# Performance work log

Measured on AMD Instinct MI355X. Metric: run time of the kernel, lower is better.

## Reference

```python
import jax, jax.numpy as jnp
import numpy as np

B = 1
NG, NM = 262144, 40962          # grid nodes, mesh nodes (icosphere level 6)
E = 131072                      # grid2mesh edges (g2m_enum)
EM, EM2 = 65536, 65536          # mesh edges / mesh2grid edges (passthrough)
GEMB = MEMB = EEMB = 128
HID1, HID2 = 512, 64
EPS = 1e-5


def setup_inputs() -> dict:
    key = jax.random.key(0)
    ks = jax.random.split(key, 16)
    inp = {
        "gx": jax.random.normal(ks[0], (B, NG, GEMB), jnp.float32),
        "mx": jax.random.normal(ks[1], (B, NM, MEMB), jnp.float32),
        "me_i": jax.random.randint(ks[2], (2, EM), 0, NM, jnp.int64 if jax.config.jax_enable_x64 else jnp.int32),
        "me_x": jax.random.normal(ks[3], (B, EM, EEMB), jnp.float32),
        "g2me_i": jnp.stack([
            jax.random.randint(ks[4], (E,), 0, NG),   # row: grid node index
            jax.random.randint(ks[5], (E,), 0, NM),   # col: mesh node index
        ]),
        "g2me_x": jax.random.normal(ks[6], (B, E, EEMB), jnp.float32),
        "m2ge_i": jax.random.randint(ks[7], (2, EM2), 0, NM),
        "m2ge_x": jax.random.normal(ks[8], (B, EM2, EEMB), jnp.float32),
    }
    # MLP params (Linear stores W as [out, in]; we keep [in, out] for x @ W)
    din = GEMB + MEMB + EEMB
    s1, s2, s3 = 1.0 / np.sqrt(din), 1.0 / np.sqrt(HID1), 1.0 / np.sqrt(HID2)
    inp["W1"] = jax.random.uniform(ks[9], (din, HID1), jnp.float32, -s1, s1)
    inp["b1"] = jax.random.uniform(ks[10], (HID1,), jnp.float32, -s1, s1)
    inp["W2"] = jax.random.uniform(ks[11], (HID1, HID2), jnp.float32, -s2, s2)
    inp["b2"] = jax.random.uniform(ks[12], (HID2,), jnp.float32, -s2, s2)
    inp["W3"] = jax.random.uniform(ks[13], (HID2, EEMB), jnp.float32, -s3, s3)
    inp["b3"] = jax.random.uniform(ks[14], (EEMB,), jnp.float32, -s3, s3)
    # LayerNorm over normalized_shape=(E, EEMB): per-(edge, channel) affine
    inp["ln_w"] = jnp.ones((E, EEMB), jnp.float32)
    inp["ln_b"] = jnp.zeros((E, EEMB), jnp.float32)
    return inp


def reference(gx, mx, me_i, me_x, g2me_i, g2me_x, m2ge_i, m2ge_x,
              W1, b1, W2, b2, W3, b3, ln_w, ln_b):
    row, col = g2me_i[0], g2me_i[1]
    # gather + concat: [B, E, gemb+memb+eemb]
    h = jnp.concatenate([gx[:, row], mx[:, col], g2me_x], axis=-1)
    h = jax.nn.silu(h @ W1 + b1)
    h = jax.nn.silu(h @ W2 + b2)
    h = h @ W3 + b3                                   # [B, E, eemb]
    # LayerNorm over BOTH edge and embed dims (normalized_shape=(E, eemb))
    mean = jnp.mean(h, axis=(-2, -1), keepdims=True)
    var = jnp.mean(jnp.square(h - mean), axis=(-2, -1), keepdims=True)
    h = (h - mean) * jax.lax.rsqrt(var + EPS) * ln_w + ln_b
    g2me_x_new = g2me_x + h
    return g2me_x_new
```

## Files before the change

kernel.cpp:

```cpp
#include <hip/hip_runtime.h>

#define NE    131072
#define DIN   384
#define DH1   512
#define DH2   64

typedef __attribute__((ext_vector_type(8))) short short8_t;
typedef __attribute__((ext_vector_type(4))) float f32x4;
typedef unsigned short ushort_t;

__device__ __forceinline__ float bf2f(ushort_t u) {
  union { unsigned int i; float f; } v; v.i = ((unsigned int)u) << 16; return v.f;
}
__device__ __forceinline__ ushort_t f2bf(float f) {
  union { float f; unsigned int i; } v; v.f = f;
  unsigned int r = v.i + 0x7fff + ((v.i >> 16) & 1);
  return (ushort_t)(r >> 16);
}
__device__ __forceinline__ float silu_f(float x) {
  return x / (1.0f + __expf(-x));
}
__device__ __forceinline__ void wave_fence() {
  __builtin_amdgcn_wave_barrier();
  asm volatile("" ::: "memory");
}

__global__ void prep_kernel(const void* __restrict__ W1, const void* __restrict__ W2,
                            const void* __restrict__ W3, const void* __restrict__ b1,
                            const void* __restrict__ b2, const void* __restrict__ b3,
                            const void* __restrict__ lnw, const void* __restrict__ g2me_raw,
                            ushort_t* __restrict__ W1f, ushort_t* __restrict__ W2f,
                            ushort_t* __restrict__ W3f, float* __restrict__ b1f,
                            float* __restrict__ b2f, float* __restrict__ b3f,
                            float* __restrict__ stats, int* __restrict__ flag,
                            int* __restrict__ idx32) {
  const int isbf = (((const ushort_t*)lnw)[0] == 0x3F80) ? 1 : 0;
  const unsigned int* gi = (const unsigned int*)g2me_raw;
  const int is64 = ((gi[1] | gi[3] | gi[5] | gi[7]) == 0) ? 1 : 0;

  int tid = blockIdx.x * blockDim.x + threadIdx.x;
  int nth = gridDim.x * blockDim.x;
  if (tid == 0) { stats[0] = 0.f; stats[1] = 0.f; *flag = isbf; }

  const ushort_t* W1u = (const ushort_t*)W1; const float* W1p = (const float*)W1;
  const ushort_t* W2u = (const ushort_t*)W2; const float* W2p = (const float*)W2;
  const ushort_t* W3u = (const ushort_t*)W3; const float* W3p = (const float*)W3;
  const ushort_t* b1u = (const ushort_t*)b1; const float* b1p = (const float*)b1;
  const ushort_t* b2u = (const ushort_t*)b2; const float* b2p = (const float*)b2;
  const ushort_t* b3u = (const ushort_t*)b3; const float* b3p = (const float*)b3;

  for (int i = tid; i < DIN * DH1; i += nth) {
    int j = i & 7, l = (i >> 3) & 63, f = i >> 9;
    int kc = f / 48, kt = (f >> 2) % 12, nt = f & 3;
    int col = kc * 64 + nt * 16 + (l & 15);
    int k   = kt * 32 + (l >> 4) * 8 + j;
    int s = k * DH1 + col;
    W1f[i] = isbf ? W1u[s] : f2bf(W1p[s]);
  }
  for (int i = tid; i < DH1 * DH2; i += nth) {
    int j = i & 7, l = (i >> 3) & 63, f = i >> 9;
    int kc = f >> 3, kt2 = (f >> 2) & 1, nt = f & 3;
    int col = nt * 16 + (l & 15);
    int k   = kc * 64 + kt2 * 32 + (l >> 4) * 8 + j;
    int s = k * DH2 + col;
    W2f[i] = isbf ? W2u[s] : f2bf(W2p[s]);
  }
  for (int i = tid; i < DH2 * 128; i += nth) {
    int j = i & 7, l = (i >> 3) & 63, f = i >> 9;
    int nt = f >> 1, kt = f & 1;
    int col = nt * 16 + (l & 15);
    int k   = kt * 32 + (l >> 4) * 8 + j;
    int s = k * 128 + col;
    W3f[i] = isbf ? W3u[s] : f2bf(W3p[s]);
  }
  for (int i = tid; i < DH1; i += nth) b1f[i] = isbf ? bf2f(b1u[i]) : b1p[i];
  for (int i = tid; i < DH2; i += nth) b2f[i] = isbf ? bf2f(b2u[i]) : b2p[i];
  for (int i = tid; i < 128; i += nth) b3f[i] = isbf ? bf2f(b3u[i]) : b3p[i];

  const long long* g64 = (const long long*)g2me_raw;
  const int* g32 = (const int*)g2me_raw;
  for (int i = tid; i < 2 * NE; i += nth)
    idx32[i] = is64 ? (int)g64[i] : g32[i];
}

template <int BF16>
__launch_bounds__(256)
__global__ void mlp_kernel(const void* __restrict__ gx_, const void* __restrict__ mx_,
                           const int* __restrict__ idx, const void* __restrict__ gex_,
                           const ushort_t* __restrict__ W1f, const float* __restrict__ b1f,
                           const ushort_t* __restrict__ W2f, const float* __restrict__ b2f,
                           const ushort_t* __restrict__ W3f, const float* __restrict__ b3f,
                           void* __restrict__ h3g_, float* __restrict__ stats,
                           const int* __restrict__ flag) {
  if (flag[0] != BF16) return;

  __shared__ __align__(16) ushort_t h1c[64][72];
  __shared__ float red[8];

  const int tid  = threadIdx.x;
  const int w    = tid >> 6;
  const int lane = tid & 63;
  const int quad = lane >> 4;
  const int c16  = lane & 15;
  const int e0   = blockIdx.x * 64;
  const int e    = e0 + w * 16 + c16;

  const int r0 = idx[e];
  const int c0 = idx[NE + e];

  short8_t afr[12];
  if (BF16) {
    const ushort_t* pg = (const ushort_t*)gx_  + (size_t)r0 * 128;
    const ushort_t* pm = (const ushort_t*)mx_  + (size_t)c0 * 128;
    const ushort_t* pe = (const ushort_t*)gex_ + (size_t)e  * 128;
    #pragma unroll
    for (int kt = 0; kt < 12; ++kt) {
      const ushort_t* p = (kt < 4) ? pg : (kt < 8) ? pm : pe;
      afr[kt] = *(const short8_t*)(p + (kt & 3) * 32 + quad * 8);
    }
  } else {
    const float* pg = (const float*)gx_  + (size_t)r0 * 128;
    const float* pm = (const float*)mx_  + (size_t)c0 * 128;
    const float* pe = (const float*)gex_ + (size_t)e  * 128;
    #pragma unroll
    for (int kt = 0; kt < 12; ++kt) {
      const float* p = ((kt < 4) ? pg : (kt < 8) ? pm : pe) + (kt & 3) * 32 + quad * 8;
      float4 u = *(const float4*)p;
      float4 v = *(const float4*)(p + 4);
      short8_t s;
      s[0] = (short)f2bf(u.x); s[1] = (short)f2bf(u.y);
      s[2] = (short)f2bf(u.z); s[3] = (short)f2bf(u.w);
      s[4] = (short)f2bf(v.x); s[5] = (short)f2bf(v.y);
      s[6] = (short)f2bf(v.z); s[7] = (short)f2bf(v.w);
      afr[kt] = s;
    }
  }

  const f32x4 vzero = {0.f, 0.f, 0.f, 0.f};
  f32x4 acc2[4];
  #pragma unroll
  for (int nt = 0; nt < 4; ++nt) acc2[nt] = vzero;

  for (int kc = 0; kc < 8; ++kc) {
    f32x4 acc1[4];
    #pragma unroll
    for (int nt = 0; nt < 4; ++nt) acc1[nt] = vzero;
    #pragma unroll
    for (int kt = 0; kt < 12; ++kt) {
      #pragma unroll
      for (int nt = 0; nt < 4; ++nt) {
        short8_t b = *(const short8_t*)(W1f + ((size_t)((kc * 12 + kt) * 4 + nt) * 64 + lane) * 8);
        acc1[nt] = __builtin_amdgcn_mfma_f32_16x16x32_bf16(afr[kt], b, acc1[nt], 0, 0, 0);
      }
    }
    #pragma unroll
    for (int nt = 0; nt < 4; ++nt) {
      float bias = b1f[kc * 64 + nt * 16 + c16];
      #pragma unroll
      for (int r = 0; r < 4; ++r) {
        float x = acc1[nt][r] + bias;
        h1c[w * 16 + quad * 4 + r][nt * 16 + c16] = f2bf(silu_f(x));
      }
    }
    wave_fence();
    #pragma unroll
    for (int kt2 = 0; kt2 < 2; ++kt2) {
      short8_t a2 = *(const short8_t*)&h1c[w * 16 + c16][kt2 * 32 + quad * 8];
      #pragma unroll
      for (int nt = 0; nt < 4; ++nt) {
        short8_t b = *(const short8_t*)(W2f + ((size_t)((kc * 2 + kt2) * 4 + nt) * 64 + lane) * 8);
        acc2[nt] = __builtin_amdgcn_mfma_f32_16x16x32_bf16(a2, b, acc2[nt], 0, 0, 0);
      }
    }
    wave_fence();
  }

  #pragma unroll
  for (int nt = 0; nt < 4; ++nt) {
    float bias = b2f[nt * 16 + c16];
    #pragma unroll
    for (int r = 0; r < 4; ++r) {
      float x = acc2[nt][r] + bias;
      h1c[w * 16 + quad * 4 + r][nt * 16 + c16] = f2bf(silu_f(x));
    }
  }
  wave_fence();
  short8_t a3[2];
  #pragma unroll
  for (int kt = 0; kt < 2; ++kt)
    a3[kt] = *(const short8_t*)&h1c[w * 16 + c16][kt * 32 + quad * 8];

  float s = 0.f, s2 = 0.f;
  #pragma unroll
  for (int nt = 0; nt < 8; ++nt) {
    f32x4 acc3 = vzero;
    #pragma unroll
    for (int kt = 0; kt < 2; ++kt) {
      short8_t b = *(const short8_t*)(W3f + ((size_t)(nt * 2 + kt) * 64 + lane) * 8);
      acc3 = __builtin_amdgcn_mfma_f32_16x16x32_bf16(a3[kt], b, acc3, 0, 0, 0);
    }
    float bias = b3f[nt * 16 + c16];
    #pragma unroll
    for (int r = 0; r < 4; ++r) {
      float v = acc3[r] + bias;
      s += v; s2 += v * v;
      size_t oidx = (size_t)(e0 + w * 16 + quad * 4 + r) * 128 + nt * 16 + c16;
      if (BF16) ((ushort_t*)h3g_)[oidx] = f2bf(v);
      else      ((float*)h3g_)[oidx] = v;
    }
  }

  #pragma unroll
  for (int off = 32; off > 0; off >>= 1) {
    s  += __shfl_xor(s, off, 64);
    s2 += __shfl_xor(s2, off, 64);
  }
  if (lane == 0) { red[w] = s; red[4 + w] = s2; }
  __syncthreads();
  if (tid == 0) {
    atomicAdd(&stats[0], red[0] + red[1] + red[2] + red[3]);
    atomicAdd(&stats[1], red[4] + red[5] + red[6] + red[7]);
  }
}

__device__ __forceinline__ unsigned int ln2(unsigned int h, unsigned int g,
                                            unsigned int wv, unsigned int bv,
                                            float mean, float inv) {
  float h0 = bf2f((ushort_t)(h & 0xffff)), h1 = bf2f((ushort_t)(h >> 16));
  float g0 = bf2f((ushort_t)(g & 0xffff)), g1 = bf2f((ushort_t)(g >> 16));
  float w0 = bf2f((ushort_t)(wv & 0xffff)), w1 = bf2f((ushort_t)(wv >> 16));
  float b0 = bf2f((ushort_t)(bv & 0xffff)), b1 = bf2f((ushort_t)(bv >> 16));
  float r0 = g0 + (h0 - mean) * inv * w0 + b0;
  float r1 = g1 + (h1 - mean) * inv * w1 + b1;
  return (unsigned int)f2bf(r0) | ((unsigned int)f2bf(r1) << 16);
}

template <int BF16>
__global__ void finalize_kernel(const void* __restrict__ gex_, const void* __restrict__ lnw_,
                                const void* __restrict__ lnb_, const float* __restrict__ stats,
                                void* __restrict__ out_, const int* __restrict__ flag) {
  if (flag[0] != BF16) return;
  const float invN = 1.0f / 16777216.0f;
  float mean = stats[0] * invN;
  float var  = stats[1] * invN - mean * mean;
  float inv  = rsqrtf(var + 1e-5f);
  size_t i = ((size_t)blockIdx.x * 256 + threadIdx.x) * 8;

  if (BF16) {
    ushort_t* out = (ushort_t*)out_;
    const ushort_t* gex = (const ushort_t*)gex_;
    const ushort_t* lnw = (const ushort_t*)lnw_;
    const ushort_t* lnb = (const ushort_t*)lnb_;
    uint4 hv = *(const uint4*)(out + i);
    uint4 gv = *(const uint4*)(gex + i);
    uint4 wv = *(const uint4*)(lnw + i);
    uint4 bv = *(const uint4*)(lnb + i);
    uint4 o;
    o.x = ln2(hv.x, gv.x, wv.x, bv.x, mean, inv);
    o.y = ln2(hv.y, gv.y, wv.y, bv.y, mean, inv);
    o.z = ln2(hv.z, gv.z, wv.z, bv.z, mean, inv);
    o.w = ln2(hv.w, gv.w, wv.w, bv.w, mean, inv);
    *(uint4*)(out + i) = o;
  } else {
    float* out = (float*)out_;
    const float* gex = (const float*)gex_;
    const float* lnw = (const float*)lnw_;
    const float* lnb = (const float*)lnb_;
    #pragma unroll
    for (int j = 0; j < 8; j += 4) {
      float4 h = *(const float4*)(out + i + j);
      float4 g = *(const float4*)(gex + i + j);
      float4 w = *(const float4*)(lnw + i + j);
      float4 b = *(const float4*)(lnb + i + j);
      float4 o;
      o.x = g.x + (h.x - mean) * inv * w.x + b.x;
      o.y = g.y + (h.y - mean) * inv * w.y + b.y;
      o.z = g.z + (h.z - mean) * inv * w.z + b.z;
      o.w = g.w + (h.w - mean) * inv * w.w + b.w;
      *(float4*)(out + i + j) = o;
    }
  }
}

extern "C" void kernel_launch(void* const* d_in, const int* in_sizes, int n_in,
                              void* d_out, int out_size, void* d_ws, size_t ws_size,
                              hipStream_t stream) {
  const void* gx     = d_in[0];
  const void* mx     = d_in[1];
  const void* g2me_i = d_in[4];
  const void* gex    = d_in[5];
  const void* W1 = d_in[8];  const void* b1 = d_in[9];
  const void* W2 = d_in[10]; const void* b2 = d_in[11];
  const void* W3 = d_in[12]; const void* b3 = d_in[13];
  const void* lnw = d_in[14]; const void* lnb = d_in[15];

  char* ws = (char*)d_ws;
  ushort_t* W1f = (ushort_t*)(ws);
  ushort_t* W2f = (ushort_t*)(ws + 393216);
  ushort_t* W3f = (ushort_t*)(ws + 458752);
  float*    b1f = (float*)(ws + 475136);
  float*    b2f = (float*)(ws + 477184);
  float*    b3f = (float*)(ws + 477440);
  float*  stats = (float*)(ws + 477952);
  int*     flag = (int*)(ws + 477960);
  int*    idx32 = (int*)(ws + 478208);

  prep_kernel<<<dim3(256), dim3(256), 0, stream>>>(
      W1, W2, W3, b1, b2, b3, lnw, g2me_i,
      W1f, W2f, W3f, b1f, b2f, b3f, stats, flag, idx32);

  mlp_kernel<0><<<dim3(NE / 64), dim3(256), 0, stream>>>(
      gx, mx, idx32, gex, W1f, b1f, W2f, b2f, W3f, b3f, d_out, stats, flag);
  mlp_kernel<1><<<dim3(NE / 64), dim3(256), 0, stream>>>(
      gx, mx, idx32, gex, W1f, b1f, W2f, b2f, W3f, b3f, d_out, stats, flag);

  finalize_kernel<0><<<dim3(8192), dim3(256), 0, stream>>>(
      gex, lnw, lnb, stats, d_out, flag);
  finalize_kernel<1><<<dim3(8192), dim3(256), 0, stream>>>(
      gex, lnw, lnb, stats, d_out, flag);
}
```

Baseline: 758.9 us.

## Process two 16-edge tiles per wave to reuse weight fragments

Each wave now handles 32 edges as two M-tiles, so every W1/W2/W3 fragment loaded from global memory feeds two MFMAs instead of one. This halves the weight-load traffic per edge, and the grid shrinks to NE/128 blocks. The prep kernel's weight swizzle loops now iterate over source indices, so reads are coalesced and writes are scattered. The cost is more registers (two sets of A fragments and accumulators), which launch_bounds(256,2) caps, and a larger shared buffer; spills or lower occupancy are possible.

Measured after the change: 642.7 us. 1.18x faster.

```diff
diff --git a/kernel.cpp b/kernel.cpp
--- a/kernel.cpp
+++ b/kernel.cpp
@@ -49,29 +49,26 @@
   const ushort_t* b2u = (const ushort_t*)b2; const float* b2p = (const float*)b2;
   const ushort_t* b3u = (const ushort_t*)b3; const float* b3p = (const float*)b3;
 
-  for (int i = tid; i < DIN * DH1; i += nth) {
-    int j = i & 7, l = (i >> 3) & 63, f = i >> 9;
-    int kc = f / 48, kt = (f >> 2) % 12, nt = f & 3;
-    int col = kc * 64 + nt * 16 + (l & 15);
-    int k   = kt * 32 + (l >> 4) * 8 + j;
-    int s = k * DH1 + col;
-    W1f[i] = isbf ? W1u[s] : f2bf(W1p[s]);
-  }
-  for (int i = tid; i < DH1 * DH2; i += nth) {
-    int j = i & 7, l = (i >> 3) & 63, f = i >> 9;
-    int kc = f >> 3, kt2 = (f >> 2) & 1, nt = f & 3;
-    int col = nt * 16 + (l & 15);
-    int k   = kc * 64 + kt2 * 32 + (l >> 4) * 8 + j;
-    int s = k * DH2 + col;
-    W2f[i] = isbf ? W2u[s] : f2bf(W2p[s]);
-  }
-  for (int i = tid; i < DH2 * 128; i += nth) {
-    int j = i & 7, l = (i >> 3) & 63, f = i >> 9;
-    int nt = f >> 1, kt = f & 1;
-    int col = nt * 16 + (l & 15);
-    int k   = kt * 32 + (l >> 4) * 8 + j;
-    int s = k * 128 + col;
-    W3f[i] = isbf ? W3u[s] : f2bf(W3p[s]);
+  for (int s = tid; s < DIN * DH1; s += nth) {
+    int k = s / DH1, col = s % DH1;
+    int c = col & 15, nt = (col >> 4) & 3, kc = col >> 6;
+    int j = k & 7, q = (k >> 3) & 3, kt = k >> 5;
+    int f = kc * 48 + kt * 4 + nt, l = q * 16 + c;
+    W1f[(f * 64 + l) * 8 + j] = isbf ? W1u[s] : f2bf(W1p[s]);
+  }
+  for (int s = tid; s < DH1 * DH2; s += nth) {
+    int k = s / DH2, col = s % DH2;
+    int c = col & 15, nt = (col >> 4) & 3;
+    int j = k & 7, q = (k >> 3) & 3, kt2 = (k >> 5) & 1, kc = k >> 6;
+    int f = kc * 8 + kt2 * 4 + nt, l = q * 16 + c;
+    W2f[(f * 64 + l) * 8 + j] = isbf ? W2u[s] : f2bf(W2p[s]);
+  }
+  for (int s = tid; s < DH2 * 128; s += nth) {
+    int k = s / 128, col = s % 128;
+    int c = col & 15, nt = col >> 4;
+    int j = k & 7, q = (k >> 3) & 3, kt = k >> 5;
+    int f = nt * 2 + kt, l = q * 16 + c;
+    W3f[(f * 64 + l) * 8 + j] = isbf ? W3u[s] : f2bf(W3p[s]);
   }
   for (int i = tid; i < DH1; i += nth) b1f[i] = isbf ? bf2f(b1u[i]) : b1p[i];
   for (int i = tid; i < DH2; i += nth) b2f[i] = isbf ? bf2f(b2u[i]) : b2p[i];
@@ -84,7 +81,7 @@
 }
 
 template <int BF16>
-__launch_bounds__(256)
+__launch_bounds__(256, 2)
 __global__ void mlp_kernel(const void* __restrict__ gx_, const void* __restrict__ mx_,
                            const int* __restrict__ idx, const void* __restrict__ gex_,
                            const ushort_t* __restrict__ W1f, const float* __restrict__ b1f,
@@ -94,7 +91,7 @@
                            const int* __restrict__ flag) {
   if (flag[0] != BF16) return;
 
-  __shared__ __align__(16) ushort_t h1c[64][72];
+  __shared__ __align__(16) ushort_t h1c[128][72];
   __shared__ float red[8];
 
   const int tid  = threadIdx.x;
@@ -102,112 +99,133 @@
   const int lane = tid & 63;
   const int quad = lane >> 4;
   const int c16  = lane & 15;
-  const int e0   = blockIdx.x * 64;
-  const int e    = e0 + w * 16 + c16;
-
-  const int r0 = idx[e];
-  const int c0 = idx[NE + e];
-
-  short8_t afr[12];
-  if (BF16) {
-    const ushort_t* pg = (const ushort_t*)gx_  + (size_t)r0 * 128;
-    const ushort_t* pm = (const ushort_t*)mx_  + (size_t)c0 * 128;
-    const ushort_t* pe = (const ushort_t*)gex_ + (size_t)e  * 128;
-    #pragma unroll
-    for (int kt = 0; kt < 12; ++kt) {
-      const ushort_t* p = (kt < 4) ? pg : (kt < 8) ? pm : pe;
-      afr[kt] = *(const short8_t*)(p + (kt & 3) * 32 + quad * 8);
-    }
-  } else {
-    const float* pg = (const float*)gx_  + (size_t)r0 * 128;
-    const float* pm = (const float*)mx_  + (size_t)c0 * 128;
-    const float* pe = (const float*)gex_ + (size_t)e  * 128;
-    #pragma unroll
-    for (int kt = 0; kt < 12; ++kt) {
-      const float* p = ((kt < 4) ? pg : (kt < 8) ? pm : pe) + (kt & 3) * 32 + quad * 8;
-      float4 u = *(const float4*)p;
-      float4 v = *(const float4*)(p + 4);
-      short8_t s;
-      s[0] = (short)f2bf(u.x); s[1] = (short)f2bf(u.y);
-      s[2] = (short)f2bf(u.z); s[3] = (short)f2bf(u.w);
-      s[4] = (short)f2bf(v.x); s[5] = (short)f2bf(v.y);
-      s[6] = (short)f2bf(v.z); s[7] = (short)f2bf(v.w);
-      afr[kt] = s;
+  const int e0   = blockIdx.x * 128;
+  const int eb   = e0 + w * 32;
+
+  short8_t afr[2][12];
+  #pragma unroll
+  for (int m = 0; m < 2; ++m) {
+    const int e  = eb + m * 16 + c16;
+    const int r0 = idx[e];
+    const int c0 = idx[NE + e];
+    if (BF16) {
+      const ushort_t* pg = (const ushort_t*)gx_  + (size_t)r0 * 128;
+      const ushort_t* pm = (const ushort_t*)mx_  + (size_t)c0 * 128;
+      const ushort_t* pe = (const ushort_t*)gex_ + (size_t)e  * 128;
+      #pragma unroll
+      for (int kt = 0; kt < 12; ++kt) {
+        const ushort_t* p = (kt < 4) ? pg : (kt < 8) ? pm : pe;
+        afr[m][kt] = *(const short8_t*)(p + (kt & 3) * 32 + quad * 8);
+      }
+    } else {
+      const float* pg = (const float*)gx_  + (size_t)r0 * 128;
+      const float* pm = (const float*)mx_  + (size_t)c0 * 128;
+      const float* pe = (const float*)gex_ + (size_t)e  * 128;
+      #pragma unroll
+      for (int kt = 0; kt < 12; ++kt) {
+        const float* p = ((kt < 4) ? pg : (kt < 8) ? pm : pe) + (kt & 3) * 32 + quad * 8;
+        float4 u = *(const float4*)p;
+        float4 v = *(const float4*)(p + 4);
+        short8_t s;
+        s[0] = (short)f2bf(u.x); s[1] = (short)f2bf(u.y);
+        s[2] = (short)f2bf(u.z); s[3] = (short)f2bf(u.w);
+        s[4] = (short)f2bf(v.x); s[5] = (short)f2bf(v.y);
+        s[6] = (short)f2bf(v.z); s[7] = (short)f2bf(v.w);
+        afr[m][kt] = s;
+      }
     }
   }
 
   const f32x4 vzero = {0.f, 0.f, 0.f, 0.f};
-  f32x4 acc2[4];
-  #pragma unroll
-  for (int nt = 0; nt < 4; ++nt) acc2[nt] = vzero;
+  f32x4 acc2[2][4];
+  #pragma unroll
+  for (int m = 0; m < 2; ++m)
+    #pragma unroll
+    for (int nt = 0; nt < 4; ++nt) acc2[m][nt] = vzero;
 
   for (int kc = 0; kc < 8; ++kc) {
-    f32x4 acc1[4];
-    #pragma unroll
-    for (int nt = 0; nt < 4; ++nt) acc1[nt] = vzero;
+    f32x4 acc1[2][4];
+    #pragma unroll
+    for (int m = 0; m < 2; ++m)
+      #pragma unroll
+      for (int nt = 0; nt < 4; ++nt) acc1[m][nt] = vzero;
     #pragma unroll
     for (int kt = 0; kt < 12; ++kt) {
       #pragma unroll
       for (int nt = 0; nt < 4; ++nt) {
         short8_t b = *(const short8_t*)(W1f + ((size_t)((kc * 12 + kt) * 4 + nt) * 64 + lane) * 8);
-        acc1[nt] = __builtin_amdgcn_mfma_f32_16x16x32_bf16(afr[kt], b, acc1[nt], 0, 0, 0);
-      }
-    }
-    #pragma unroll
-    for (int nt = 0; nt < 4; ++nt) {
-      float bias = b1f[kc * 64 + nt * 16 + c16];
-      #pragma unroll
-      for (int r = 0; r < 4; ++r) {
-        float x = acc1[nt][r] + bias;
-        h1c[w * 16 + quad * 4 + r][nt * 16 + c16] = f2bf(silu_f(x));
-      }
-    }
+        acc1[0][nt] = __builtin_amdgcn_mfma_f32_16x16x32_bf16(afr[0][kt], b, acc1[0][nt], 0, 0, 0);
+        acc1[1][nt] = __builtin_amdgcn_mfma_f32_16x16x32_bf16(afr[1][kt], b, acc1[1][nt], 0, 0, 0);
+      }
+    }
+    #pragma unroll
+    for (int m = 0; m < 2; ++m)
+      #pragma unroll
+      for (int nt = 0; nt < 4; ++nt) {
+        float bias = b1f[kc * 64 + nt * 16 + c16];
+        #pragma unroll
+        for (int r = 0; r < 4; ++r) {
+          float x = acc1[m][nt][r] + bias;
+          h1c[w * 32 + m * 16 + quad * 4 + r][nt * 16 + c16] = f2bf(silu_f(x));
+        }
+      }
     wave_fence();
     #pragma unroll
     for (int kt2 = 0; kt2 < 2; ++kt2) {
-      short8_t a2 = *(const short8_t*)&h1c[w * 16 + c16][kt2 * 32 + quad * 8];
+      short8_t a2[2];
+      #pragma unroll
+      for (int m = 0; m < 2; ++m)
+        a2[m] = *(const short8_t*)&h1c[w * 32 + m * 16 + c16][kt2 * 32 + quad * 8];
       #pragma unroll
       for (int nt = 0; nt < 4; ++nt) {
         short8_t b = *(const short8_t*)(W2f + ((size_t)((kc * 2 + kt2) * 4 + nt) * 64 + lane) * 8);
-        acc2[nt] = __builtin_amdgcn_mfma_f32_16x16x32_bf16(a2, b, acc2[nt], 0, 0, 0);
+        acc2[0][nt] = __builtin_amdgcn_mfma_f32_16x16x32_bf16(a2[0], b, acc2[0][nt], 0, 0, 0);
+        acc2[1][nt] = __builtin_amdgcn_mfma_f32_16x16x32_bf16(a2[1], b, acc2[1][nt], 0, 0, 0);
       }
     }
     wave_fence();
   }
 
   #pragma unroll
-  for (int nt = 0; nt < 4; ++nt) {
-    float bias = b2f[nt * 16 + c16];
-    #pragma unroll
-    for (int r = 0; r < 4; ++r) {
-      float x = acc2[nt][r] + bias;
-      h1c[w * 16 + quad * 4 + r][nt * 16 + c16] = f2bf(silu_f(x));
-    }
-  }
+  for (int m = 0; m < 2; ++m)
+    #pragma unroll
+    for (int nt = 0; nt < 4; ++nt) {
+      float bias = b2f[nt * 16 + c16];
+      #pragma unroll
+      for (int r = 0; r < 4; ++r) {
+        float x = acc2[m][nt][r] + bias;
+        h1c[w * 32 + m * 16 + quad * 4 + r][nt * 16 + c16] = f2bf(silu_f(x));
+      }
+    }
   wave_fence();
-  short8_t a3[2];
-  #pragma unroll
-  for (int kt = 0; kt < 2; ++kt)
-    a3[kt] = *(const short8_t*)&h1c[w * 16 + c16][kt * 32 + quad * 8];
+  short8_t a3[2][2];
+  #pragma unroll
+  for (int m = 0; m < 2; ++m)
+    #pragma unroll
+    for (int kt = 0; kt < 2; ++kt)
+      a3[m][kt] = *(const short8_t*)&h1c[w * 32 + m * 16 + c16][kt * 32 + quad * 8];
 
   float s = 0.f, s2 = 0.f;
   #pragma unroll
   for (int nt = 0; nt < 8; ++nt) {
-    f32x4 acc3 = vzero;
+    f32x4 acc3[2] = {vzero, vzero};
     #pragma unroll
     for (int kt = 0; kt < 2; ++kt) {
       short8_t b = *(const short8_t*)(W3f + ((size_t)(nt * 2 + kt) * 64 + lane) * 8);
-      acc3 = __builtin_amdgcn_mfma_f32_16x16x32_bf16(a3[kt], b, acc3, 0, 0, 0);
+      acc3[0] = __builtin_amdgcn_mfma_f32_16x16x32_bf16(a3[0][kt], b, acc3[0], 0, 0, 0);
+      acc3[1] = __builtin_amdgcn_mfma_f32_16x16x32_bf16(a3[1][kt], b, acc3[1], 0, 0, 0);
     }
     float bias = b3f[nt * 16 + c16];
     #pragma unroll
-    for (int r = 0; r < 4; ++r) {
-      float v = acc3[r] + bias;
-      s += v; s2 += v * v;
-      size_t oidx = (size_t)(e0 + w * 16 + quad * 4 + r) * 128 + nt * 16 + c16;
-      if (BF16) ((ushort_t*)h3g_)[oidx] = f2bf(v);
-      else      ((float*)h3g_)[oidx] = v;
-    }
+    for (int m = 0; m < 2; ++m)
+      #pragma unroll
+      for (int r = 0; r < 4; ++r) {
+        float v = acc3[m][r] + bias;
+        s += v; s2 += v * v;
+        size_t oidx = (size_t)(eb + m * 16 + quad * 4 + r) * 128 + nt * 16 + c16;
+        if (BF16) ((ushort_t*)h3g_)[oidx] = f2bf(v);
+        else      ((float*)h3g_)[oidx] = v;
+      }
   }
 
   #pragma unroll
@@ -309,9 +327,9 @@
       W1, W2, W3, b1, b2, b3, lnw, g2me_i,
       W1f, W2f, W3f, b1f, b2f, b3f, stats, flag, idx32);
 
-  mlp_kernel<0><<<dim3(NE / 64), dim3(256), 0, stream>>>(
+  mlp_kernel<0><<<dim3(NE / 128), dim3(256), 0, stream>>>(
       gx, mx, idx32, gex, W1f, b1f, W2f, b2f, W3f, b3f, d_out, stats, flag);
-  mlp_kernel<1><<<dim3(NE / 64), dim3(256), 0, stream>>>(
+  mlp_kernel<1><<<dim3(NE / 128), dim3(256), 0, stream>>>(
       gx, mx, idx32, gex, W1f, b1f, W2f, b2f, W3f, b3f, d_out, stats, flag);
 
   finalize_kernel<0><<<dim3(8192), dim3(256), 0, stream>>>(
```
